# Optimization experiments

Measured on AMD Instinct MI355X. Metric: run time of the kernel, lower is better.

## Reference

```python
import math
import jax, jax.numpy as jnp
import numpy as np

B, T, C = 4, 2048, 1024
H = 16
HS = C // H  # head_size = 64

def setup_inputs() -> dict:
    key = jax.random.key(0)
    k1, k2, k3 = jax.random.split(key, 3)
    x = jax.random.normal(k1, (B, T, C), dtype=jnp.float32)
    W_qkv = jax.random.normal(k2, (C, 3 * C), dtype=jnp.float32) * (1.0 / math.sqrt(C))
    W_proj = jax.random.normal(k3, (C, C), dtype=jnp.float32) * (1.0 / math.sqrt(C))
    b_proj = jnp.zeros((C,), dtype=jnp.float32)
    return {"x": x, "W_qkv": W_qkv, "W_proj": W_proj, "b_proj": b_proj}

def reference(x, W_qkv, W_proj, b_proj):
    Bx, Tx, Cx = x.shape
    qkv = x @ W_qkv  # [B,T,3C]
    q, k, v = jnp.split(qkv, 3, axis=-1)
    # [B,T,C] -> [B,H,T,HS]
    def heads(t):
        return t.reshape(Bx, Tx, H, HS).transpose(0, 2, 1, 3)
    q, k, v = heads(q), heads(k), heads(v)
    scores = jnp.einsum('bhqd,bhkd->bhqk', q, k) / math.sqrt(HS)
    causal = jnp.tril(jnp.ones((Tx, Tx), dtype=bool))
    scores = jnp.where(causal, scores, -jnp.inf)
    attn = jax.nn.softmax(scores, axis=-1)
    out = jnp.einsum('bhqk,bhkd->bhqd', attn, v)  # [B,H,T,HS]
    out = out.transpose(0, 2, 1, 3).reshape(Bx, Tx, Cx)
    return out @ W_proj + b_proj
```

## Files before the change

### kernel.cpp

```cpp
#include <hip/hip_runtime.h>
#include <hip/hip_bf16.h>
#include <cstdint>
#include <cstddef>

using bf16 = __hip_bfloat16;
typedef __attribute__((ext_vector_type(8))) short short8;
typedef __attribute__((ext_vector_type(4))) float floatx4;

#define B_ 4
#define T_ 2048
#define C_ 1024
#define H_ 16
#define HS_ 64
#define BT_ (B_*T_)
#define N3C (3*C_)

#define MFMA16(a,b,c) __builtin_amdgcn_mfma_f32_16x16x32_bf16((a),(b),(c),0,0,0)

#if __has_builtin(__builtin_amdgcn_exp2f)
#define EXP2(x) __builtin_amdgcn_exp2f(x)
#else
#define EXP2(x) exp2f(x)
#endif

static __device__ __forceinline__ void gld16(const bf16* g, bf16* l) {
  __builtin_amdgcn_global_load_lds(
      (const __attribute__((address_space(1))) unsigned int*)g,
      (__attribute__((address_space(3))) unsigned int*)l, 16, 0, 0);
}

static __device__ __forceinline__ unsigned short f2bf_us(float x) {
  bf16 b = __float2bfloat16(x);
  return *(unsigned short*)&b;
}

__global__ __launch_bounds__(256)
void k_prep(const float* __restrict__ x, bf16* __restrict__ xb,
            const float* __restrict__ Wqkv, bf16* __restrict__ wqkvT,
            const float* __restrict__ Wproj, bf16* __restrict__ wprojT)
{
  const int bid = blockIdx.x, tid = threadIdx.x;
  __shared__ float tile[64][65];

  if (bid < 4096) {
    const int i = bid*256 + tid;
    const float4 v0 = ((const float4*)x)[2*i];
    const float4 v1 = ((const float4*)x)[2*i + 1];
    union { bf16 b[8]; uint4 u; } cvt;
    cvt.b[0] = __float2bfloat16(v0.x);
    cvt.b[1] = __float2bfloat16(v0.y);
    cvt.b[2] = __float2bfloat16(v0.z);
    cvt.b[3] = __float2bfloat16(v0.w);
    cvt.b[4] = __float2bfloat16(v1.x);
    cvt.b[5] = __float2bfloat16(v1.y);
    cvt.b[6] = __float2bfloat16(v1.z);
    cvt.b[7] = __float2bfloat16(v1.w);
    ((uint4*)xb)[i] = cvt.u;
    return;
  }

  const float* in; bf16* out; int N, n0, k0;
  if (bid < 4864) {
    const int j = bid - 4096;
    in = Wqkv; out = wqkvT; N = N3C;
    n0 = (j % 48) * 64; k0 = (j / 48) * 64;
  } else {
    const int j = bid - 4864;
    in = Wproj; out = wprojT; N = C_;
    n0 = (j % 16) * 64; k0 = (j / 16) * 64;
  }
  const int r = tid >> 6, c = tid & 63;
  #pragma unroll
  for (int j = 0; j < 16; ++j)
    tile[r + j*4][c] = in[(size_t)(k0 + r + j*4) * N + n0 + c];
  __syncthreads();
  #pragma unroll
  for (int j = 0; j < 16; ++j) {
    int rr = r + j*4;
    out[(size_t)(n0 + rr) * C_ + k0 + c] = __float2bfloat16(tile[c][rr]);
  }
}

template<int MODE, int NB>
__global__ __launch_bounds__(256, 2)
void k_gemm(const bf16* __restrict__ A, const bf16* __restrict__ Bt,
            int N, int K,
            bf16* __restrict__ Qb, bf16* __restrict__ Kb, bf16* __restrict__ Vt,
            float* __restrict__ Out, const float* __restrict__ bias)
{
  __shared__ __align__(16) char smem[65536];
  bf16* const sAb = (bf16*)smem;
  bf16* const sBb = (bf16*)(smem + 32768);

  const int tid  = threadIdx.x;
  const int lane = tid & 63, wave = tid >> 6;
  const int quad = lane >> 4, l16 = lane & 15;
  const int wm = wave >> 1, wn = wave & 1;

  const int g = blockIdx.x;
  const int xcd = g & 7;
  const int local = g >> 3;
  const int nb = local % NB;
  const int mb = (local / NB) * 8 + xcd;
  const int m0 = mb * 128, n0 = nb * 128;

  const int ra = tid >> 3;
  const int gc = (tid & 7) ^ (ra & 7);
  const bf16* aptr = A  + (size_t)(m0 + ra) * K + gc*8;
  const bf16* bptr = Bt + (size_t)(n0 + ra) * K + gc*8;
  const size_t rj = (size_t)32 * K;

  floatx4 acc[4][4] = {};
  const int KI = K >> 6;
  const int x7a = l16 & 7;

  for (int i = 0; i <= KI; ++i) {
    __syncthreads();
    if (i < KI) {
      const int k0 = i << 6;
      bf16* sa = sAb + (i & 1) * 8192;
      bf16* sb = sBb + (i & 1) * 8192;
      #pragma unroll
      for (int q2 = 0; q2 < 4; ++q2) {
        gld16(aptr + q2*rj + k0, sa + q2*2048 + tid*8);
        gld16(bptr + q2*rj + k0, sb + q2*2048 + tid*8);
      }
    }
    if (i == 0) continue;
    const bf16* sa = sAb + ((i-1) & 1) * 8192;
    const bf16* sb = sBb + ((i-1) & 1) * 8192;
    #pragma unroll
    for (int ks = 0; ks < 2; ++ks) {
      short8 af[4], bfm[4];
      #pragma unroll
      for (int ii = 0; ii < 4; ++ii)
        af[ii] = *(const short8*)&sa[(wm*64 + ii*16 + l16)*64 + ((ks*4 + quad) ^ x7a)*8];
      #pragma unroll
      for (int ii = 0; ii < 4; ++ii)
        bfm[ii] = *(const short8*)&sb[(wn*64 + ii*16 + l16)*64 + ((ks*4 + quad) ^ x7a)*8];
      #pragma unroll
      for (int ii = 0; ii < 4; ++ii)
        #pragma unroll
        for (int j = 0; j < 4; ++j)
          acc[ii][j] = MFMA16(af[ii], bfm[j], acc[ii][j]);
    }
  }

  if (MODE == 0 && nb >= 16) {
    __syncthreads();
    unsigned short* epi = (unsigned short*)smem;
    #pragma unroll
    for (int i = 0; i < 4; ++i) {
      const int tl = wm*64 + i*16 + quad*4;
      #pragma unroll
      for (int j = 0; j < 4; ++j) {
        const int ccl = wn*64 + j*16 + l16;
        #pragma unroll
        for (int r = 0; r < 4; ++r)
          epi[ccl*132 + tl + r] = f2bf_us(acc[i][j][r]);
      }
    }
    __syncthreads();
    const int b  = m0 >> 11;
    const int t0 = m0 & 2047;
    const int h0 = (n0 - 2*C_) >> 6;
    #pragma unroll
    for (int it = 0; it < 32; ++it) {
      const int id = it*256 + tid;
      const int tp = id & 31;
      const int rest = id >> 5;
      const int tl64 = (rest & 1) * 64;
      const int ccl = rest >> 1;
      const int k0p = tp + (tp & 16);
      const unsigned lo = epi[ccl*132 + tl64 + k0p];
      const unsigned hi = epi[ccl*132 + tl64 + k0p + 16];
      const int h = h0 + (ccl >> 6), d = ccl & 63;
      unsigned* row = (unsigned*)(Vt + ((size_t)(b*H_ + h) * HS_ + d) * T_);
      row[(t0 >> 1) + tl64/2 + tp] = lo | (hi << 16);
    }
  } else {
    #pragma unroll
    for (int i = 0; i < 4; ++i) {
      const int rowb = m0 + wm*64 + i*16 + quad*4;
      #pragma unroll
      for (int j = 0; j < 4; ++j) {
        const int col = n0 + wn*64 + j*16 + l16;
        #pragma unroll
        for (int r = 0; r < 4; ++r) {
          const float v = acc[i][j][r];
          const int rr = rowb + r;
          if (MODE == 0) {
            const int b = rr >> 11, t = rr & 2047;
            const int h = (col >> 6) & 15, d = col & 63;
            const size_t addr = (((size_t)(b*H_ + h) * T_ + t) << 6) + d;
            if (nb < 8) {
              Qb[addr] = __float2bfloat16(v * 0.18033688f);
            } else {
              Kb[addr] = __float2bfloat16(v);
            }
          } else {
            Out[(size_t)rr * N + col] = v + bias[col];
          }
        }
      }
    }
  }
}

__global__ __launch_bounds__(256, 3)
void k_attn(const bf16* __restrict__ Q, const bf16* __restrict__ K,
            const bf16* __restrict__ Vt, bf16* __restrict__ att)
{
  __shared__ bf16 kbuf[2][64*64];
  __shared__ bf16 vbuf[2][64*64];
  __shared__ bf16 pbuf[4][32*64];

  const int tid  = threadIdx.x;
  const int lane = tid & 63, wave = tid >> 6;
  const int quad = lane >> 4, l16 = lane & 15;
  const int x7 = l16 & 7;

  const int g  = blockIdx.x;
  const int bh = (g & 7) * 8 + ((g >> 3) & 7);
  const int qt = 15 - (g >> 6);
  const int b = bh >> 4, h = bh & 15;

  const bf16* Qp = Q  + (size_t)bh * T_ * HS_;
  const bf16* Kp = K  + (size_t)bh * T_ * HS_;
  const bf16* Vp = Vt + (size_t)bh * HS_ * T_;

  const int qbase = qt*128 + wave*32;
  const int ntk = 2*qt + 2;

  short8 qf[2][2];
  #pragma unroll
  for (int mt = 0; mt < 2; ++mt)
    #pragma unroll
    for (int ss = 0; ss < 2; ++ss)
      qf[mt][ss] = *(const short8*)(Qp + (size_t)(qbase + mt*16 + l16) * HS_ + ss*32 + quad*8);

  floatx4 o[2][4] = {};
  float lrow[2][4] = {};

  const bf16* kg[2]; const bf16* vg[2];
  int ldsoff[2];
  #pragma unroll
  for (int it = 0; it < 2; ++it) {
    const int c = it*256 + tid;
    const int row = c >> 3;
    const int col = (c & 7) ^ (row & 7);
    kg[it] = Kp + (size_t)row * HS_ + col*8;
    vg[it] = Vp + (size_t)row * T_ + col*8;
    ldsoff[it] = c*8;
  }

  bf16* pw = pbuf[wave];
  unsigned int* pw32 = (unsigned int*)pw;
  const int c0 = l16 >> 2;
  const int dwl = l16 & 3;

  for (int i = 0; i <= ntk; ++i) {
    __syncthreads();
    if (i < ntk) {
      const int stk0 = i * 64;
      bf16* kb = kbuf[i & 1];
      bf16* vb = vbuf[i & 1];
      #pragma unroll
      for (int it = 0; it < 2; ++it) {
        gld16(kg[it] + (size_t)stk0 * HS_, kb + ldsoff[it]);
        gld16(vg[it] + stk0,               vb + ldsoff[it]);
      }
    }
    if (i == 0) continue;
    const int tk  = i - 1;
    const int tk0 = tk * 64;
    if (tk0 > qbase + 31) continue;
    const bf16* kb = kbuf[tk & 1];
    const bf16* vb = vbuf[tk & 1];

    floatx4 s[2][4] = {};
    __builtin_amdgcn_s_setprio(1);
    #pragma unroll
    for (int nt = 0; nt < 4; ++nt) {
      const int key = nt*16 + l16;
      #pragma unroll
      for (int ss = 0; ss < 2; ++ss) {
        short8 kf = *(const short8*)&kb[(key*8 + ((ss*4+quad) ^ x7))*8];
        s[0][nt] = MFMA16(qf[0][ss], kf, s[0][nt]);
        s[1][nt] = MFMA16(qf[1][ss], kf, s[1][nt]);
      }
    }
    __builtin_amdgcn_s_setprio(0);

    if (tk0 + 63 > qbase) {
      #pragma unroll
      for (int mt = 0; mt < 2; ++mt)
        #pragma unroll
        for (int nt = 0; nt < 4; ++nt) {
          const int key = tk0 + nt*16 + l16;
          #pragma unroll
          for (int r = 0; r < 4; ++r) {
            const int qr = qbase + mt*16 + quad*4 + r;
            if (key > qr) s[mt][nt][r] = -1e30f;
          }
        }
    }

    #pragma unroll
    for (int mt = 0; mt < 2; ++mt) {
      #pragma unroll
      for (int r = 0; r < 4; ++r) {
        const float p0 = EXP2(s[mt][0][r]), p1 = EXP2(s[mt][1][r]);
        const float p2 = EXP2(s[mt][2][r]), p3 = EXP2(s[mt][3][r]);
        lrow[mt][r] += (p0 + p1) + (p2 + p3);
        const int q = mt*16 + quad*4 + r;
        const unsigned w0 = __builtin_amdgcn_perm(__float_as_uint(p1), __float_as_uint(p0), 0x07060302u);
        const unsigned w1 = __builtin_amdgcn_perm(__float_as_uint(p3), __float_as_uint(p2), 0x07060302u);
        pw32[q*32 + (((c0 + q)     & 7) << 2) + dwl] = w0;
        pw32[q*32 + (((c0 + q + 4) & 7) << 2) + dwl] = w1;
      }
    }

    __builtin_amdgcn_s_setprio(1);
    #pragma unroll
    for (int ss = 0; ss < 2; ++ss) {
      short8 pf0 = *(const short8*)&pw[l16*64      + ((4*ss + quad + l16) & 7)*8];
      short8 pf1 = *(const short8*)&pw[(16+l16)*64 + ((4*ss + quad + l16) & 7)*8];
      #pragma unroll
      for (int nd = 0; nd < 4; ++nd) {
        const int d = nd*16 + l16;
        short8 vf = *(const short8*)&vb[(d*8 + ((ss*4+quad) ^ x7))*8];
        o[0][nd] = MFMA16(pf0, vf, o[0][nd]);
        o[1][nd] = MFMA16(pf1, vf, o[1][nd]);
      }
    }
    __builtin_amdgcn_s_setprio(0);
  }

  #pragma unroll
  for (int mt = 0; mt < 2; ++mt) {
    #pragma unroll
    for (int r = 0; r < 4; ++r) {
      float lsum = lrow[mt][r];
      lsum += __shfl_xor(lsum, 1);
      lsum += __shfl_xor(lsum, 2);
      lsum += __shfl_xor(lsum, 4);
      lsum += __shfl_xor(lsum, 8);
      const float inv = 1.0f / lsum;
      const int tt = qbase + mt*16 + quad*4 + r;
      #pragma unroll
      for (int nd = 0; nd < 4; ++nd)
        att[(size_t)(b*T_ + tt) * C_ + h*64 + nd*16 + l16] =
            __float2bfloat16(o[mt][nd][r] * inv);
    }
  }
}

extern "C" void kernel_launch(void* const* d_in, const int* in_sizes, int n_in,
                              void* d_out, int out_size, void* d_ws, size_t ws_size,
                              hipStream_t stream) {
  const float* x     = (const float*)d_in[0];
  const float* Wqkv  = (const float*)d_in[1];
  const float* Wproj = (const float*)d_in[2];
  const float* bproj = (const float*)d_in[3];
  float* out = (float*)d_out;

  char* ws = (char*)d_ws;
  bf16* xb     = (bf16*)(ws + 0);
  bf16* wqkvT  = (bf16*)(ws + 16777216);
  bf16* wprojT = (bf16*)(ws + 23068672);
  bf16* Qb     = (bf16*)(ws + 25165824);
  bf16* Kb     = (bf16*)(ws + 41943040);
  bf16* Vt     = (bf16*)(ws + 58720256);
  bf16* att    = (bf16*)(ws + 75497472);

  k_prep<<<dim3(5120), 256, 0, stream>>>(x, xb, Wqkv, wqkvT, Wproj, wprojT);
  k_gemm<0, 24><<<dim3(1536), 256, 0, stream>>>(
      xb, wqkvT, N3C, C_, Qb, Kb, Vt, nullptr, nullptr);
  k_attn<<<dim3(1024), 256, 0, stream>>>(Qb, Kb, Vt, att);
  k_gemm<1, 8><<<dim3(512), 256, 0, stream>>>(
      att, wprojT, C_, C_, nullptr, nullptr, nullptr, out, bproj);
}
```

Measured before the change: 232.1 us.

## Use 256x256-tile 8-wave GEMM kernel for QKV projection

Replaces the 128x128-tile QKV GEMM with a dedicated 512-thread kernel that computes 256x256 output tiles using BK=32 double-buffered LDS, swizzled loads, and s_setprio around MFMA bursts. Larger tiles raise arithmetic intensity and cut global/L2 traffic per FLOP, and the grid shrinks to 384 blocks mapped across XCDs. The V-transpose epilogue is done in four passes through LDS to fit the 256-wide tile. Risks include lower occupancy (1 block/CU), tail imbalance with 384 blocks on 256 CUs, and more barriers per k-step.

After: 239.9 us. 1.03x slower.

```diff
diff --git a/kernel.cpp b/kernel.cpp
--- a/kernel.cpp
+++ b/kernel.cpp
@@ -81,6 +81,143 @@
   }
 }
 
+__global__ __launch_bounds__(512, 1)
+void k_gemm256(const bf16* __restrict__ A, const bf16* __restrict__ Bt,
+               bf16* __restrict__ Qb, bf16* __restrict__ Kb, bf16* __restrict__ Vt)
+{
+  __shared__ __align__(16) char smem[65536];
+  bf16* const sA = (bf16*)smem;
+  bf16* const sB = (bf16*)(smem + 32768);
+
+  const int tid  = threadIdx.x;
+  const int lane = tid & 63, wave = tid >> 6;
+  const int quad = lane >> 4, l16 = lane & 15;
+  const int wm = wave >> 2, wn = wave & 3;
+
+  const int g = blockIdx.x;
+  const int xcd = g & 7;
+  const int local = g >> 3;
+  const int nb = local % 12;
+  const int mb = (local / 12) * 8 + xcd;
+  const int m0 = mb * 256, n0 = nb * 256;
+
+  const int ra = tid >> 2;
+  const int gc = (tid & 3) ^ (ra & 3);
+  const bf16* aptr = A  + (size_t)(m0 + ra) * C_ + gc*8;
+  const bf16* bptr = Bt + (size_t)(n0 + ra) * C_ + gc*8;
+
+  floatx4 acc[8][4] = {};
+  const int aoff = (wm*128 + l16)*32 + (quad ^ (l16 & 3))*8;
+  const int boff = (wn*64  + l16)*32 + (quad ^ (l16 & 3))*8;
+
+  gld16(aptr,            sA + tid*8);
+  gld16(aptr + 128*C_,   sA + 4096 + tid*8);
+  gld16(bptr,            sB + tid*8);
+  gld16(bptr + 128*C_,   sB + 4096 + tid*8);
+
+  for (int i = 0; i < 32; ++i) {
+    const int cur = i & 1;
+    if (i + 1 < 32) {
+      const int k0 = (i + 1) * 32;
+      bf16* sa = sA + (cur ^ 1) * 8192;
+      bf16* sb = sB + (cur ^ 1) * 8192;
+      gld16(aptr + k0,           sa + tid*8);
+      gld16(aptr + 128*C_ + k0,  sa + 4096 + tid*8);
+      gld16(bptr + k0,           sb + tid*8);
+      gld16(bptr + 128*C_ + k0,  sb + 4096 + tid*8);
+      asm volatile("s_waitcnt vmcnt(4)" ::: "memory");
+    } else {
+      asm volatile("s_waitcnt vmcnt(0)" ::: "memory");
+    }
+    asm volatile("s_barrier" ::: "memory");
+    const bf16* sa = sA + cur * 8192;
+    const bf16* sb = sB + cur * 8192;
+    short8 a0[4], bq[4], a1[4];
+    #pragma unroll
+    for (int ii = 0; ii < 4; ++ii) a0[ii] = *(const short8*)&sa[aoff + ii*512];
+    #pragma unroll
+    for (int j = 0; j < 4; ++j)   bq[j]  = *(const short8*)&sb[boff + j*512];
+    __builtin_amdgcn_s_setprio(1);
+    #pragma unroll
+    for (int ii = 0; ii < 4; ++ii)
+      #pragma unroll
+      for (int j = 0; j < 4; ++j)
+        acc[ii][j] = MFMA16(a0[ii], bq[j], acc[ii][j]);
+    __builtin_amdgcn_s_setprio(0);
+    #pragma unroll
+    for (int ii = 0; ii < 4; ++ii) a1[ii] = *(const short8*)&sa[aoff + 2048 + ii*512];
+    asm volatile("s_barrier" ::: "memory");
+    __builtin_amdgcn_s_setprio(1);
+    #pragma unroll
+    for (int ii = 0; ii < 4; ++ii)
+      #pragma unroll
+      for (int j = 0; j < 4; ++j)
+        acc[4+ii][j] = MFMA16(a1[ii], bq[j], acc[4+ii][j]);
+    __builtin_amdgcn_s_setprio(0);
+    asm volatile("s_barrier" ::: "memory");
+  }
+
+  if (nb >= 8) {
+    unsigned short* epi = (unsigned short*)smem;
+    const int b  = m0 >> 11;
+    const int t0 = m0 & 2047;
+    #pragma unroll 1
+    for (int pass = 0; pass < 4; ++pass) {
+      if (wn == pass) {
+        #pragma unroll
+        for (int ii = 0; ii < 8; ++ii) {
+          const int tl = wm*128 + ii*16 + quad*4;
+          #pragma unroll
+          for (int j = 0; j < 4; ++j) {
+            const int ccl = j*16 + l16;
+            #pragma unroll
+            for (int r = 0; r < 4; ++r)
+              epi[ccl*264 + tl + r] = f2bf_us(acc[ii][j][r]);
+          }
+        }
+      }
+      __syncthreads();
+      const int h = ((n0 - 2*C_) >> 6) + pass;
+      #pragma unroll
+      for (int it = 0; it < 16; ++it) {
+        const int id = it*512 + tid;
+        const int tp = id & 31;
+        const int rest = id >> 5;
+        const int tl64 = (rest & 3) * 64;
+        const int ccl = rest >> 2;
+        const int k0p = tp + (tp & 16);
+        const unsigned lo = epi[ccl*264 + tl64 + k0p];
+        const unsigned hi = epi[ccl*264 + tl64 + k0p + 16];
+        unsigned* row = (unsigned*)(Vt + ((size_t)(b*H_ + h) * HS_ + ccl) * T_);
+        row[(t0 >> 1) + tl64/2 + tp] = lo | (hi << 16);
+      }
+      if (pass < 3) __syncthreads();
+    }
+  } else {
+    #pragma unroll
+    for (int ii = 0; ii < 8; ++ii) {
+      const int rowb = m0 + wm*128 + ii*16 + quad*4;
+      #pragma unroll
+      for (int j = 0; j < 4; ++j) {
+        const int col = n0 + wn*64 + j*16 + l16;
+        const int h = (col >> 6) & 15, d = col & 63;
+        #pragma unroll
+        for (int r = 0; r < 4; ++r) {
+          const float v = acc[ii][j][r];
+          const int rr = rowb + r;
+          const int bb = rr >> 11, t = rr & 2047;
+          const size_t addr = (((size_t)(bb*H_ + h) * T_ + t) << 6) + d;
+          if (nb < 4) {
+            Qb[addr] = __float2bfloat16(v * 0.18033688f);
+          } else {
+            Kb[addr] = __float2bfloat16(v);
+          }
+        }
+      }
+    }
+  }
+}
+
 template<int MODE, int NB>
 __global__ __launch_bounds__(256, 2)
 void k_gemm(const bf16* __restrict__ A, const bf16* __restrict__ Bt,
@@ -146,61 +283,18 @@
     }
   }
 
-  if (MODE == 0 && nb >= 16) {
-    __syncthreads();
-    unsigned short* epi = (unsigned short*)smem;
-    #pragma unroll
-    for (int i = 0; i < 4; ++i) {
-      const int tl = wm*64 + i*16 + quad*4;
-      #pragma unroll
-      for (int j = 0; j < 4; ++j) {
-        const int ccl = wn*64 + j*16 + l16;
-        #pragma unroll
-        for (int r = 0; r < 4; ++r)
-          epi[ccl*132 + tl + r] = f2bf_us(acc[i][j][r]);
-      }
-    }
-    __syncthreads();
-    const int b  = m0 >> 11;
-    const int t0 = m0 & 2047;
-    const int h0 = (n0 - 2*C_) >> 6;
-    #pragma unroll
-    for (int it = 0; it < 32; ++it) {
-      const int id = it*256 + tid;
-      const int tp = id & 31;
-      const int rest = id >> 5;
-      const int tl64 = (rest & 1) * 64;
-      const int ccl = rest >> 1;
-      const int k0p = tp + (tp & 16);
-      const unsigned lo = epi[ccl*132 + tl64 + k0p];
-      const unsigned hi = epi[ccl*132 + tl64 + k0p + 16];
-      const int h = h0 + (ccl >> 6), d = ccl & 63;
-      unsigned* row = (unsigned*)(Vt + ((size_t)(b*H_ + h) * HS_ + d) * T_);
-      row[(t0 >> 1) + tl64/2 + tp] = lo | (hi << 16);
-    }
-  } else {
-    #pragma unroll
-    for (int i = 0; i < 4; ++i) {
-      const int rowb = m0 + wm*64 + i*16 + quad*4;
-      #pragma unroll
-      for (int j = 0; j < 4; ++j) {
-        const int col = n0 + wn*64 + j*16 + l16;
-        #pragma unroll
-        for (int r = 0; r < 4; ++r) {
-          const float v = acc[i][j][r];
-          const int rr = rowb + r;
-          if (MODE == 0) {
-            const int b = rr >> 11, t = rr & 2047;
-            const int h = (col >> 6) & 15, d = col & 63;
-            const size_t addr = (((size_t)(b*H_ + h) * T_ + t) << 6) + d;
-            if (nb < 8) {
-              Qb[addr] = __float2bfloat16(v * 0.18033688f);
-            } else {
-              Kb[addr] = __float2bfloat16(v);
-            }
-          } else {
-            Out[(size_t)rr * N + col] = v + bias[col];
-          }
+  #pragma unroll
+  for (int i = 0; i < 4; ++i) {
+    const int rowb = m0 + wm*64 + i*16 + quad*4;
+    #pragma unroll
+    for (int j = 0; j < 4; ++j) {
+      const int col = n0 + wn*64 + j*16 + l16;
+      #pragma unroll
+      for (int r = 0; r < 4; ++r) {
+        const float v = acc[i][j][r];
+        const int rr = rowb + r;
+        if (MODE == 1) {
+          Out[(size_t)rr * N + col] = v + bias[col];
         }
       }
     }
@@ -375,8 +469,7 @@
   bf16* att    = (bf16*)(ws + 75497472);
 
   k_prep<<<dim3(5120), 256, 0, stream>>>(x, xb, Wqkv, wqkvT, Wproj, wprojT);
-  k_gemm<0, 24><<<dim3(1536), 256, 0, stream>>>(
-      xb, wqkvT, N3C, C_, Qb, Kb, Vt, nullptr, nullptr);
+  k_gemm256<<<dim3(384), 512, 0, stream>>>(xb, wqkvT, Qb, Kb, Vt);
   k_attn<<<dim3(1024), 256, 0, stream>>>(Qb, Kb, Vt, att);
   k_gemm<1, 8><<<dim3(512), 256, 0, stream>>>(
       att, wprojT, C_, C_, nullptr, nullptr, nullptr, out, bproj);
```

## Deepen GEMM k-loop to four-stage shared-memory pipeline with BK=32

Applied to the files above, without the earlier changes.

Restructures the bf16 GEMM main loop from a double-buffered BK=64 scheme into a four-slot ring of BK=32 stages, with three tiles prefetched ahead. Explicit vmcnt waits plus a raw s_barrier replace the full __syncthreads, and the LDS swizzle is changed for 32-wide rows. s_setprio is raised around the MFMA block. The aim is to hide global-load latency better and cut barrier stalls, at the cost of more loop iterations and hand-managed waitcnt correctness.

After: 226.7 us. 2.3% less time.

```diff
diff --git a/kernel.cpp b/kernel.cpp
--- a/kernel.cpp
+++ b/kernel.cpp
@@ -89,8 +89,8 @@
             float* __restrict__ Out, const float* __restrict__ bias)
 {
   __shared__ __align__(16) char smem[65536];
-  bf16* const sAb = (bf16*)smem;
-  bf16* const sBb = (bf16*)(smem + 32768);
+  bf16* const sA = (bf16*)smem;
+  bf16* const sB = (bf16*)(smem + 32768);
 
   const int tid  = threadIdx.x;
   const int lane = tid & 63, wave = tid >> 6;
@@ -104,46 +104,55 @@
   const int mb = (local / NB) * 8 + xcd;
   const int m0 = mb * 128, n0 = nb * 128;
 
-  const int ra = tid >> 3;
-  const int gc = (tid & 7) ^ (ra & 7);
+  const int ra = tid >> 2;
+  const int gc = (tid & 3) ^ ((ra >> 1) & 3);
   const bf16* aptr = A  + (size_t)(m0 + ra) * K + gc*8;
   const bf16* bptr = Bt + (size_t)(n0 + ra) * K + gc*8;
-  const size_t rj = (size_t)32 * K;
-
+  const size_t rj = (size_t)64 * K;
+
+  const int KT = K >> 5;
   floatx4 acc[4][4] = {};
-  const int KI = K >> 6;
-  const int x7a = l16 & 7;
-
-  for (int i = 0; i <= KI; ++i) {
-    __syncthreads();
-    if (i < KI) {
-      const int k0 = i << 6;
-      bf16* sa = sAb + (i & 1) * 8192;
-      bf16* sb = sBb + (i & 1) * 8192;
-      #pragma unroll
-      for (int q2 = 0; q2 < 4; ++q2) {
-        gld16(aptr + q2*rj + k0, sa + q2*2048 + tid*8);
-        gld16(bptr + q2*rj + k0, sb + q2*2048 + tid*8);
-      }
-    }
-    if (i == 0) continue;
-    const bf16* sa = sAb + ((i-1) & 1) * 8192;
-    const bf16* sb = sBb + ((i-1) & 1) * 8192;
-    #pragma unroll
-    for (int ks = 0; ks < 2; ++ks) {
-      short8 af[4], bfm[4];
-      #pragma unroll
-      for (int ii = 0; ii < 4; ++ii)
-        af[ii] = *(const short8*)&sa[(wm*64 + ii*16 + l16)*64 + ((ks*4 + quad) ^ x7a)*8];
-      #pragma unroll
-      for (int ii = 0; ii < 4; ++ii)
-        bfm[ii] = *(const short8*)&sb[(wn*64 + ii*16 + l16)*64 + ((ks*4 + quad) ^ x7a)*8];
-      #pragma unroll
-      for (int ii = 0; ii < 4; ++ii)
-        #pragma unroll
-        for (int j = 0; j < 4; ++j)
-          acc[ii][j] = MFMA16(af[ii], bfm[j], acc[ii][j]);
-    }
+  const int swz = (l16 >> 1) & 3;
+  const int aoff = (wm*64 + l16)*32 + (quad ^ swz)*8;
+  const int boff = (wn*64 + l16)*32 + (quad ^ swz)*8;
+
+  #pragma unroll
+  for (int t = 0; t < 3; ++t) {
+    bf16* sa = sA + t*4096; bf16* sb = sB + t*4096;
+    gld16(aptr + t*32,      sa + tid*8);
+    gld16(aptr + rj + t*32, sa + 2048 + tid*8);
+    gld16(bptr + t*32,      sb + tid*8);
+    gld16(bptr + rj + t*32, sb + 2048 + tid*8);
+  }
+
+  #pragma unroll 1
+  for (int i = 0; i < KT; ++i) {
+    if (i < KT-2)       asm volatile("s_waitcnt vmcnt(8)" ::: "memory");
+    else if (i == KT-2) asm volatile("s_waitcnt vmcnt(4)" ::: "memory");
+    else                asm volatile("s_waitcnt vmcnt(0)" ::: "memory");
+    asm volatile("s_barrier" ::: "memory");
+    if (i < KT-3) {
+      const int t = i + 3;
+      bf16* sa = sA + (t & 3)*4096; bf16* sb = sB + (t & 3)*4096;
+      gld16(aptr + t*32,      sa + tid*8);
+      gld16(aptr + rj + t*32, sa + 2048 + tid*8);
+      gld16(bptr + t*32,      sb + tid*8);
+      gld16(bptr + rj + t*32, sb + 2048 + tid*8);
+    }
+    const bf16* sa = sA + (i & 3)*4096;
+    const bf16* sb = sB + (i & 3)*4096;
+    short8 af[4], bfm[4];
+    #pragma unroll
+    for (int ii = 0; ii < 4; ++ii) af[ii]  = *(const short8*)&sa[aoff + ii*512];
+    #pragma unroll
+    for (int j = 0; j < 4; ++j)    bfm[j]  = *(const short8*)&sb[boff + j*512];
+    __builtin_amdgcn_s_setprio(1);
+    #pragma unroll
+    for (int ii = 0; ii < 4; ++ii)
+      #pragma unroll
+      for (int j = 0; j < 4; ++j)
+        acc[ii][j] = MFMA16(af[ii], bfm[j], acc[ii][j]);
+    __builtin_amdgcn_s_setprio(0);
   }
 
   if (MODE == 0 && nb >= 16) {
```
